# Performance work log

Hardware: AMD Instinct MI355X
Metric: run time of the kernel (lower is better)

The kernel has to match this reference:

```python
import jax, jax.numpy as jnp
import numpy as np

B, T, C, H = 4, 2048, 1024, 16
HS = C // H  # head dim = 64
EPS = 1e-5


def _layernorm(h, w, b):
    m = jnp.mean(h, axis=-1, keepdims=True)
    v = jnp.mean(jnp.square(h - m), axis=-1, keepdims=True)
    return (h - m) * jax.lax.rsqrt(v + EPS) * w + b


def _quantize_int8(t):
    # per-tensor absmax int8 quantization, matching the torch code
    absmax = jnp.max(jnp.abs(t))
    scale = jnp.where(absmax > 0, absmax / 127.0, jnp.float32(1.0))
    q = jnp.clip(jnp.round(t / scale), -127, 127).astype(jnp.int8)
    return q, scale


def setup_inputs() -> dict:
    key = jax.random.key(0)
    ks = jax.random.split(key, 8)
    w = lambda k, shape: (jax.random.normal(k, shape, jnp.float32) * 0.02)
    return {
        "x": jax.random.normal(ks[0], (B, T, C), jnp.float32),
        "ln1_w": jnp.ones((C,), jnp.float32),
        "ln1_b": jnp.zeros((C,), jnp.float32),
        "W_qkv": w(ks[1], (C, 3 * C)),
        "b_qkv": jnp.zeros((3 * C,), jnp.float32),
        "W_o": w(ks[2], (C, C)),
        "b_o": jnp.zeros((C,), jnp.float32),
        "ln2_w": jnp.ones((C,), jnp.float32),
        "ln2_b": jnp.zeros((C,), jnp.float32),
        "W_fc": w(ks[3], (C, 4 * C)),
        "b_fc": jnp.zeros((4 * C,), jnp.float32),
        "W_pr": w(ks[4], (4 * C, C)),
        "b_pr": jnp.zeros((C,), jnp.float32),
    }


def reference(x, ln1_w, ln1_b, W_qkv, b_qkv, W_o, b_o, ln2_w, ln2_b, W_fc, b_fc, W_pr, b_pr):
    # ---- attention (prefill, cache-owner, kv_cache_quant=True, use_cache=True) ----
    h = _layernorm(x, ln1_w, ln1_b)
    qkv = h @ W_qkv + b_qkv                       # (B,T,3C)
    q, k, v = jnp.split(qkv, 3, axis=-1)
    q = q.reshape(B, T, H, HS).transpose(0, 2, 1, 3)  # (B,H,T,hs)
    k = k.reshape(B, T, H, HS).transpose(0, 2, 1, 3)
    v = v.reshape(B, T, H, HS).transpose(0, 2, 1, 3)

    # quantized `present` cache (returned, not used for attention in prefill path)
    k_quant, k_scale = _quantize_int8(k)
    v_quant, v_scale = _quantize_int8(v)

    # causal SDPA (dropout=0)
    att = jnp.einsum("bhqd,bhkd->bhqk", q, k) * (1.0 / np.sqrt(HS))
    causal = jnp.tril(jnp.ones((T, T), bool))
    att = jnp.where(causal[None, None], att, jnp.float32(-jnp.inf))
    att = jax.nn.softmax(att, axis=-1)
    y = jnp.einsum("bhqk,bhkd->bhqd", att, v)
    y = y.transpose(0, 2, 1, 3).reshape(B, T, C)
    y = y @ W_o + b_o
    x = x + y

    # ---- MLP ----
    h2 = _layernorm(x, ln2_w, ln2_b)
    h2 = jax.nn.gelu(h2 @ W_fc + b_fc, approximate=False)
    x = x + (h2 @ W_pr + b_pr)

    return x, k_quant, k_scale, v_quant, v_scale
```

## Files before the change

kernel.cpp:

```cpp
#include <hip/hip_runtime.h>
#include <cmath>

typedef __bf16 bf16;
typedef float f32x4 __attribute__((ext_vector_type(4)));
typedef __bf16 bf16x4 __attribute__((ext_vector_type(4)));
typedef __bf16 bf16x8 __attribute__((ext_vector_type(8)));

#define DEVI __device__ __forceinline__

constexpr int Bn = 4, Tn = 2048, Cn = 1024, Hn = 16, HSn = 64;
constexpr int C3n = 3 * Cn;
constexpr int BTn = Bn * Tn;

constexpr size_t OFF_WT_QKV = 0;
constexpr size_t OFF_WT_O   = 6291456;
constexpr size_t OFF_WT_FC  = 8388608;
constexpr size_t OFF_WT_PR  = 16777216;
constexpr size_t OFF_H      = 25165824;
constexpr size_t OFF_Y      = 41943040;
constexpr size_t OFF_X1     = 58720256;
constexpr size_t OFF_AMAX   = 92274688;
constexpr size_t OFF_QKV    = 92274944;
constexpr size_t OFF_G      = OFF_QKV;

constexpr size_t OUT_X  = 0;
constexpr size_t OUT_KQ = 8388608;
constexpr size_t OUT_KS = 16777216;
constexpr size_t OUT_VQ = 16777217;
constexpr size_t OUT_VS = 25165825;

DEVI void g2l16(const void* g, void* l) {
  __builtin_amdgcn_global_load_lds(
      (__attribute__((address_space(1))) void*)g,
      (__attribute__((address_space(3))) void*)l, 16, 0, 0);
}

DEVI float gelu_f(float x) {
  const float ax = fabsf(x) * 0.7071067811865476f;
  const float t = 1.0f / (1.0f + 0.3275911f * ax);
  const float p = t * (0.254829592f + t * (-0.284496736f +
                  t * (1.421413741f + t * (-1.453152027f + t * 1.061405429f))));
  float er = 1.0f - p * __expf(-ax * ax);
  er = (x < 0.0f) ? -er : er;
  return 0.5f * x * (1.0f + er);
}

__global__ __launch_bounds__(256) void k_transpose(const float* __restrict__ W,
                                                   bf16* __restrict__ Wt,
                                                   int K, int N) {
  __shared__ float tile[32][33];
  const int n0 = blockIdx.x * 32, k0 = blockIdx.y * 32;
  const int tx = threadIdx.x, ty = threadIdx.y;
#pragma unroll
  for (int i = 0; i < 4; ++i) {
    int k = k0 + ty + i * 8;
    tile[ty + i * 8][tx] = W[(size_t)k * N + (n0 + tx)];
  }
  __syncthreads();
#pragma unroll
  for (int i = 0; i < 4; ++i) {
    int n = n0 + ty + i * 8;
    Wt[(size_t)n * K + (k0 + tx)] = (bf16)tile[tx][ty + i * 8];
  }
}

__global__ __launch_bounds__(256) void k_ln(const float* __restrict__ x,
                                            const float* __restrict__ g,
                                            const float* __restrict__ b,
                                            bf16* __restrict__ out) {
  __shared__ float red[8];
  const int row = blockIdx.x, tid = threadIdx.x;
  const int lane = tid & 63, wv = tid >> 6;
  f32x4 v = ((const f32x4*)(x + (size_t)row * Cn))[tid];

  float s = v[0] + v[1] + v[2] + v[3];
  s += __shfl_down(s, 32); s += __shfl_down(s, 16); s += __shfl_down(s, 8);
  s += __shfl_down(s, 4);  s += __shfl_down(s, 2);  s += __shfl_down(s, 1);
  if (!lane) red[wv] = s;
  __syncthreads();
  const float mean = (red[0] + red[1] + red[2] + red[3]) * (1.0f / 1024.0f);
  __syncthreads();

  f32x4 d = v - mean;
  float s2 = d[0]*d[0] + d[1]*d[1] + d[2]*d[2] + d[3]*d[3];
  s2 += __shfl_down(s2, 32); s2 += __shfl_down(s2, 16); s2 += __shfl_down(s2, 8);
  s2 += __shfl_down(s2, 4);  s2 += __shfl_down(s2, 2);  s2 += __shfl_down(s2, 1);
  if (!lane) red[wv] = s2;
  __syncthreads();
  const float var = (red[0] + red[1] + red[2] + red[3]) * (1.0f / 1024.0f);
  const float inv = rsqrtf(var + 1e-5f);

  f32x4 gw = ((const f32x4*)g)[tid];
  f32x4 bb = ((const f32x4*)b)[tid];
  bf16x4 o;
#pragma unroll
  for (int j = 0; j < 4; ++j) o[j] = (bf16)(d[j] * inv * gw[j] + bb[j]);
  *(bf16x4*)(out + (size_t)row * Cn + tid * 4) = o;
}

#define VMBAR(N) asm volatile("s_waitcnt vmcnt(" #N ")\n\ts_barrier" ::: "memory")
#define BARW()   asm volatile("s_barrier" ::: "memory")

DEVI void stage_half(const bf16* __restrict__ G, int ldk, int row0, int k0,
                     bf16* dst, int w, int lane) {
  const int srow = lane >> 3;
  const int sch = ((lane & 7) ^ srow) * 8;
  const bf16* src = G + (size_t)(row0 + srow) * ldk + k0 + sch;
#pragma unroll
  for (int i = 0; i < 2; ++i) {
    const int g = 2 * w + i;
    g2l16(src + (size_t)(8 * g) * ldk, dst + g * 512);
  }
}

DEVI void read_b(const bf16* BsB, int wn, int l15, int quad, bf16x8 (&bv)[4][2]) {
#pragma unroll
  for (int nt = 0; nt < 4; ++nt)
#pragma unroll
    for (int kk = 0; kk < 2; ++kk) {
      const int row = wn * 64 + nt * 16 + l15;
      const int c = ((kk * 4 + quad) ^ (l15 & 7)) * 8;
      bv[nt][kk] = *(const bf16x8*)(BsB + row * 64 + c);
    }
}

template <int MR, int Q>
DEVI void read_aq(const bf16* AsB, int wm, int l15, int quad, bf16x8 (&af)[MR][2]) {
#pragma unroll
  for (int r = 0; r < MR; ++r)
#pragma unroll
    for (int kk = 0; kk < 2; ++kk) {
      const int row = wm * (MR * 64) + (Q * MR + r) * 16 + l15;
      const int c = ((kk * 4 + quad) ^ (l15 & 7)) * 8;
      af[r][kk] = *(const bf16x8*)(AsB + row * 64 + c);
    }
}

template <int MR, int MF, int Q>
DEVI void mfma_q(const bf16x8 (&af)[MR][2], const bf16x8 (&bv)[4][2],
                 f32x4 (&acc)[MF][4]) {
  __builtin_amdgcn_s_setprio(1);
#pragma unroll
  for (int r = 0; r < MR; ++r)
#pragma unroll
    for (int nt = 0; nt < 4; ++nt)
#pragma unroll
      for (int kk = 0; kk < 2; ++kk)
        acc[Q * MR + r][nt] = __builtin_amdgcn_mfma_f32_16x16x32_bf16(
            af[r][kk], bv[nt][kk], acc[Q * MR + r][nt], 0, 0, 0);
  __builtin_amdgcn_s_setprio(0);
}

template <int BM, bool RES, bool GELU, bool AMAX, bool F32OUT>
__global__ __launch_bounds__(512, 2) void k_gemm256(const bf16* __restrict__ A,
                                                    const bf16* __restrict__ Bt,
                                                    const float* __restrict__ bias,
                                                    const float* __restrict__ res,
                                                    void* __restrict__ Cout,
                                                    unsigned int* __restrict__ amax,
                                                    int M, int N, int K) {
  constexpr int MR = BM / 128;
  constexpr int MF = BM / 32;
  __shared__ bf16 As[2][BM * 64];
  __shared__ bf16 Bs[2][256 * 64];
  __shared__ float redA[8];
  const int tid = threadIdx.x;
  const int lane = tid & 63, w = tid >> 6;
  const int wm = w >> 2, wn = w & 3;
  const int l15 = lane & 15, quad = lane >> 4;
  const int m0 = blockIdx.x * BM, n0 = blockIdx.y * 256;
  const int kIters = K >> 6, kLast = kIters - 1;
  (void)M;

#pragma unroll
  for (int hA = 0; hA < MR; ++hA)
    stage_half(A, K, m0 + 128 * hA, 0, As[0] + 8192 * hA, w, lane);
  stage_half(Bt, K, n0 + 0,   0,  Bs[0] + 0,    w, lane);
  stage_half(Bt, K, n0 + 128, 0,  Bs[0] + 8192, w, lane);
  stage_half(Bt, K, n0 + 0,   64, Bs[1] + 0,    w, lane);
  stage_half(Bt, K, n0 + 128, 64, Bs[1] + 8192, w, lane);

  f32x4 acc[MF][4] = {};

  for (int kt = 0; kt < kIters; ++kt) {
    const bf16* AsB = As[kt & 1];
    const bf16* BsB = Bs[kt & 1];
    bf16* AsN = As[(kt & 1) ^ 1];
    bf16* BsC = Bs[kt & 1];
    const bool stA = (kt + 1 < kIters);
    const bool stB = (kt + 2 < kIters);
    bf16x8 bv[4][2];
    bf16x8 af[MR][2];

    if (kt == kLast) { VMBAR(0); } else { VMBAR(4); }
    read_b(BsB, wn, l15, quad, bv);
    read_aq<MR, 0>(AsB, wm, l15, quad, af);
    if (stA) stage_half(A, K, m0 + 0, (kt + 1) * 64, AsN + 0, w, lane);
    mfma_q<MR, MF, 0>(af, bv, acc);

    BARW();
    read_aq<MR, 1>(AsB, wm, l15, quad, af);
    if constexpr (BM == 256) {
      if (stA) stage_half(A, K, m0 + 128, (kt + 1) * 64, AsN + 8192, w, lane);
    }
    mfma_q<MR, MF, 1>(af, bv, acc);

    BARW();
    read_aq<MR, 2>(AsB, wm, l15, quad, af);
    if (stB) stage_half(Bt, K, n0 + 0, (kt + 2) * 64, BsC + 0, w, lane);
    mfma_q<MR, MF, 2>(af, bv, acc);

    BARW();
    read_aq<MR, 3>(AsB, wm, l15, quad, af);
    if (stB) stage_half(Bt, K, n0 + 128, (kt + 2) * 64, BsC + 8192, w, lane);
    mfma_q<MR, MF, 3>(af, bv, acc);
  }

  const int colB = n0 + wn * 64 + l15;
  const int rowB = m0 + wm * (BM / 2) + (quad << 2);
  float lm = 0.0f;
#pragma unroll
  for (int mt = 0; mt < MF; ++mt) {
#pragma unroll
    for (int nt = 0; nt < 4; ++nt) {
      const int col = colB + nt * 16;
      const float bval = bias[col];
#pragma unroll
      for (int r = 0; r < 4; ++r) {
        const int row = rowB + mt * 16 + r;
        float val = acc[mt][nt][r] + bval;
        if (GELU) val = gelu_f(val);
        if (RES)  val += res[(size_t)row * N + col];
        if (AMAX) lm = fmaxf(lm, fabsf(val));
        if (F32OUT) ((float*)Cout)[(size_t)row * N + col] = val;
        else        ((bf16*)Cout)[(size_t)row * N + col] = (bf16)val;
      }
    }
  }

  if (AMAX) {
    const int cls = n0 >> 10;
    if (cls > 0) {
      lm = fmaxf(lm, __shfl_xor(lm, 1));
      lm = fmaxf(lm, __shfl_xor(lm, 2));
      lm = fmaxf(lm, __shfl_xor(lm, 4));
      lm = fmaxf(lm, __shfl_xor(lm, 8));
      lm = fmaxf(lm, __shfl_xor(lm, 16));
      lm = fmaxf(lm, __shfl_xor(lm, 32));
      if (!lane) redA[w] = lm;
      __syncthreads();
      if (tid == 0) {
        float m8 = redA[0];
#pragma unroll
        for (int i = 1; i < 8; ++i) m8 = fmaxf(m8, redA[i]);
        atomicMax(amax + (cls - 1), __float_as_uint(m8));
      }
    }
  }
}

__global__ __launch_bounds__(256) void k_init(unsigned int* amax) {
  if (threadIdx.x < 2) amax[threadIdx.x] = 0u;
}

__global__ __launch_bounds__(256) void k_quant(const bf16* __restrict__ qkv,
                                               const unsigned int* __restrict__ amax,
                                               float* __restrict__ out) {
  const float ka = __uint_as_float(amax[0]);
  const float va = __uint_as_float(amax[1]);
  const float ks = ka > 0.0f ? ka / 127.0f : 1.0f;
  const float vs = va > 0.0f ? va / 127.0f : 1.0f;
  if (blockIdx.x == 0 && threadIdx.x == 0) { out[OUT_KS] = ks; out[OUT_VS] = vs; }
  const float kinv = 1.0f / ks, vinv = 1.0f / vs;
  const size_t nchunks = 1048576;
  const size_t stride = (size_t)gridDim.x * blockDim.x;
  for (size_t ci = (size_t)blockIdx.x * blockDim.x + threadIdx.x; ci < nchunks; ci += stride) {
    const int d0 = (int)(ci & 7) * 8;
    const int t  = (int)(ci >> 3) & 2047;
    const int h  = (int)(ci >> 14) & 15;
    const int b  = (int)(ci >> 18);
    const size_t src = ((size_t)(b * Tn + t)) * C3n + h * HSn + d0;
    bf16x8 k8 = *(const bf16x8*)(qkv + src + Cn);
    bf16x8 v8 = *(const bf16x8*)(qkv + src + 2 * Cn);
    float kq[8], vq[8];
#pragma unroll
    for (int j = 0; j < 8; ++j) {
      kq[j] = fminf(fmaxf(rintf((float)k8[j] * kinv), -127.0f), 127.0f);
      vq[j] = fminf(fmaxf(rintf((float)v8[j] * vinv), -127.0f), 127.0f);
    }
    const size_t oi = ci * 8;
    f32x4 a0 = {kq[0], kq[1], kq[2], kq[3]};
    f32x4 a1 = {kq[4], kq[5], kq[6], kq[7]};
    *(f32x4*)(out + OUT_KQ + oi)     = a0;
    *(f32x4*)(out + OUT_KQ + oi + 4) = a1;
    float* vdst = out + OUT_VQ + oi;
#pragma unroll
    for (int j = 0; j < 8; ++j) vdst[j] = vq[j];
  }
}

__global__ __launch_bounds__(256, 3) void k_attn(const bf16* __restrict__ qkv,
                                                 bf16* __restrict__ y) {
  __shared__ bf16 Ks[2][64 * 64];
  __shared__ bf16 Vt[2][64 * 64];
  __shared__ bf16 Pt[4][2][16 * 64];

  const int tid = threadIdx.x;
  const int lane = tid & 63;
  const int w = tid >> 6;
  const int quad = lane >> 4;
  const int l15 = lane & 15;

  const int bh = blockIdx.x;
  const int qt = 15 - (int)blockIdx.y;
  const int b = bh >> 4, h = bh & 15;
  const int q0 = qt * 128;
  const int ktMax = 2 * qt + 1;

  const bf16* qkv_b = qkv + (size_t)b * Tn * C3n + h * HSn;
  const bf16* kbase = qkv_b + Cn;
  const bf16* vbase = qkv_b + 2 * Cn;

  const int srow = lane >> 3;
  const int schunk = ((lane & 7) ^ srow) * 8;

  const bf16* q0p = qkv_b + (size_t)(q0 + 16 * w + l15) * C3n;
  const bf16* q1p = q0p + (size_t)64 * C3n;
  bf16x8 qf[2][2];
  qf[0][0] = *(const bf16x8*)(q0p + quad * 8);
  qf[0][1] = *(const bf16x8*)(q0p + 32 + quad * 8);
  qf[1][0] = *(const bf16x8*)(q1p + quad * 8);
  qf[1][1] = *(const bf16x8*)(q1p + 32 + quad * 8);

  g2l16(kbase + (size_t)(8 * w + srow) * C3n + schunk, (bf16*)Ks[0] + w * 512);
  g2l16(kbase + (size_t)(8 * (w + 4) + srow) * C3n + schunk, (bf16*)Ks[0] + (w + 4) * 512);
  bf16x8 v0 = *(const bf16x8*)(vbase + (size_t)lane * C3n + w * 8);
  bf16x8 v1 = *(const bf16x8*)(vbase + (size_t)lane * C3n + (w + 4) * 8);
  __builtin_amdgcn_s_waitcnt(0);
#pragma unroll
  for (int j = 0; j < 8; ++j) {
    Vt[0][(w * 8 + j) * 64 + ((srow ^ j) << 3) + (lane & 7)] = v0[j];
    Vt[0][((w + 4) * 8 + j) * 64 + ((srow ^ j) << 3) + (lane & 7)] = v1[j];
  }
  __syncthreads();

  f32x4 Od[2][4] = {};
  float m_i[2] = {-INFINITY, -INFINITY};
  float l_i[2] = {0.0f, 0.0f};

  for (int kt = 0; kt <= ktMax; ++kt) {
    const int bsel = kt & 1;

    bf16x8 nv0, nv1;
    if (kt < ktMax) {
      const int kv1 = (kt + 1) * 64;
      g2l16(kbase + (size_t)(kv1 + 8 * w + srow) * C3n + schunk,
            (bf16*)Ks[bsel ^ 1] + w * 512);
      g2l16(kbase + (size_t)(kv1 + 8 * (w + 4) + srow) * C3n + schunk,
            (bf16*)Ks[bsel ^ 1] + (w + 4) * 512);
      nv0 = *(const bf16x8*)(vbase + (size_t)(kv1 + lane) * C3n + w * 8);
      nv1 = *(const bf16x8*)(vbase + (size_t)(kv1 + lane) * C3n + (w + 4) * 8);
    }

    const bf16* KsB = Ks[bsel];
    f32x4 S0[4] = {}, S1[4] = {};
#pragma unroll
    for (int ks = 0; ks < 2; ++ks)
#pragma unroll
      for (int nt = 0; nt < 4; ++nt) {
        const int rn = nt * 16 + l15;
        const int c = ((ks * 4 + quad) ^ (l15 & 7)) * 8;
        bf16x8 kf = *(const bf16x8*)(KsB + rn * 64 + c);
        S0[nt] = __builtin_amdgcn_mfma_f32_16x16x32_bf16(kf, qf[0][ks], S0[nt], 0, 0, 0);
        S1[nt] = __builtin_amdgcn_mfma_f32_16x16x32_bf16(kf, qf[1][ks], S1[nt], 0, 0, 0);
      }

    const int qloc = 16 * w + l15;
    const int th[2] = { kt < 2 * qt ? 64 : (kt == 2 * qt ? qloc : -1),
                        kt < ktMax ? 64 : qloc };
    f32x4* Sg[2] = {S0, S1};
#pragma unroll
    for (int g = 0; g < 2; ++g) {
      float s[4][4];
      float mx = -INFINITY;
#pragma unroll
      for (int nt = 0; nt < 4; ++nt)
#pragma unroll
        for (int r = 0; r < 4; ++r) {
          float v = Sg[g][nt][r] * 0.125f;
          if (nt * 16 + quad * 4 + r > th[g]) v = -INFINITY;
          s[nt][r] = v;
          mx = fmaxf(mx, v);
        }
      mx = fmaxf(mx, __shfl_xor(mx, 16));
      mx = fmaxf(mx, __shfl_xor(mx, 32));
      const float mn = fmaxf(m_i[g], mx);
      const float al = __expf(m_i[g] - mn);
      m_i[g] = mn;
      float rsum = 0.0f;
      bf16x4 pk[4];
#pragma unroll
      for (int nt = 0; nt < 4; ++nt)
#pragma unroll
        for (int r = 0; r < 4; ++r) {
          const float p = __expf(s[nt][r] - mn);
          rsum += p;
          pk[nt][r] = (bf16)p;
        }
      rsum += __shfl_xor(rsum, 16);
      rsum += __shfl_xor(rsum, 32);
      l_i[g] = l_i[g] * al + rsum;
#pragma unroll
      for (int dt = 0; dt < 4; ++dt) Od[g][dt] *= al;
#pragma unroll
      for (int nt = 0; nt < 4; ++nt) {
        const int phys = (nt * 2 + (quad >> 1)) ^ (l15 & 7);
        *(bf16x4*)(&Pt[w][g][0] + l15 * 64 + phys * 8 + (quad & 1) * 4) = pk[nt];
      }
    }

    const bf16* VtB = Vt[bsel];
#pragma unroll
    for (int ks2 = 0; ks2 < 2; ++ks2) {
      const int pc = ((ks2 * 4 + quad) ^ (l15 & 7)) * 8;
      bf16x8 pf0 = *(const bf16x8*)(&Pt[w][0][0] + l15 * 64 + pc);
      bf16x8 pf1 = *(const bf16x8*)(&Pt[w][1][0] + l15 * 64 + pc);
#pragma unroll
      for (int dt = 0; dt < 4; ++dt) {
        const int d = dt * 16 + l15;
        bf16x8 vf = *(const bf16x8*)(VtB + d * 64 + pc);
        Od[0][dt] = __builtin_amdgcn_mfma_f32_16x16x32_bf16(vf, pf0, Od[0][dt], 0, 0, 0);
        Od[1][dt] = __builtin_amdgcn_mfma_f32_16x16x32_bf16(vf, pf1, Od[1][dt], 0, 0, 0);
      }
    }

    if (kt < ktMax) {
      __builtin_amdgcn_s_waitcnt(0);
#pragma unroll
      for (int j = 0; j < 8; ++j) {
        Vt[bsel ^ 1][(w * 8 + j) * 64 + ((srow ^ j) << 3) + (lane & 7)] = nv0[j];
        Vt[bsel ^ 1][((w + 4) * 8 + j) * 64 + ((srow ^ j) << 3) + (lane & 7)] = nv1[j];
      }
      __syncthreads();
    }
  }

#pragma unroll
  for (int g = 0; g < 2; ++g) {
    const float invl = 1.0f / l_i[g];
    const size_t yb = ((size_t)b * Tn + q0 + g * 64 + 16 * w + l15) * Cn + h * HSn;
#pragma unroll
    for (int dt = 0; dt < 4; ++dt) {
      bf16x4 o;
#pragma unroll
      for (int r = 0; r < 4; ++r) o[r] = (bf16)(Od[g][dt][r] * invl);
      *(bf16x4*)(y + yb + dt * 16 + quad * 4) = o;
    }
  }
}

extern "C" void kernel_launch(void* const* d_in, const int* in_sizes, int n_in,
                              void* d_out, int out_size, void* d_ws, size_t ws_size,
                              hipStream_t stream) {
  const float* x     = (const float*)d_in[0];
  const float* ln1w  = (const float*)d_in[1];
  const float* ln1b  = (const float*)d_in[2];
  const float* Wqkv  = (const float*)d_in[3];
  const float* bqkv  = (const float*)d_in[4];
  const float* Wo    = (const float*)d_in[5];
  const float* bo    = (const float*)d_in[6];
  const float* ln2w  = (const float*)d_in[7];
  const float* ln2b  = (const float*)d_in[8];
  const float* Wfc   = (const float*)d_in[9];
  const float* bfc   = (const float*)d_in[10];
  const float* Wpr   = (const float*)d_in[11];
  const float* bpr   = (const float*)d_in[12];

  char* ws = (char*)d_ws;
  bf16*  Wt_qkv = (bf16*)(ws + OFF_WT_QKV);
  bf16*  Wt_o   = (bf16*)(ws + OFF_WT_O);
  bf16*  Wt_fc  = (bf16*)(ws + OFF_WT_FC);
  bf16*  Wt_pr  = (bf16*)(ws + OFF_WT_PR);
  bf16*  h      = (bf16*)(ws + OFF_H);
  bf16*  ybf    = (bf16*)(ws + OFF_Y);
  float* x1     = (float*)(ws + OFF_X1);
  unsigned int* amax = (unsigned int*)(ws + OFF_AMAX);
  bf16*  qkvbf  = (bf16*)(ws + OFF_QKV);
  bf16*  g      = (bf16*)(ws + OFF_G);
  float* out    = (float*)d_out;

  const dim3 tb(32, 8);
  k_transpose<<<dim3(96, 32),  tb, 0, stream>>>(Wqkv, Wt_qkv, 1024, 3072);
  k_transpose<<<dim3(32, 32),  tb, 0, stream>>>(Wo,   Wt_o,   1024, 1024);
  k_transpose<<<dim3(128, 32), tb, 0, stream>>>(Wfc,  Wt_fc,  1024, 4096);
  k_transpose<<<dim3(32, 128), tb, 0, stream>>>(Wpr,  Wt_pr,  4096, 1024);
  k_init<<<1, 64, 0, stream>>>(amax);

  k_ln<<<BTn, 256, 0, stream>>>(x, ln1w, ln1b, h);
  k_gemm256<256, false, false, true, false><<<dim3(32, 12), 512, 0, stream>>>(
      h, Wt_qkv, bqkv, nullptr, qkvbf, amax, 8192, 3072, 1024);
  k_quant<<<2048, 256, 0, stream>>>(qkvbf, amax, out);
  k_attn<<<dim3(64, 16), 256, 0, stream>>>(qkvbf, ybf);
  k_gemm256<128, true, false, false, true><<<dim3(64, 4), 512, 0, stream>>>(
      ybf, Wt_o, bo, x, x1, nullptr, 8192, 1024, 1024);
  k_ln<<<BTn, 256, 0, stream>>>(x1, ln2w, ln2b, h);
  k_gemm256<256, false, true, false, false><<<dim3(32, 16), 512, 0, stream>>>(
      h, Wt_fc, bfc, nullptr, g, nullptr, 8192, 4096, 1024);
  k_gemm256<128, true, false, false, true><<<dim3(64, 4), 512, 0, stream>>>(
      g, Wt_pr, bpr, x1, out, nullptr, 8192, 1024, 4096);
}
```

Before: 546.5 us.

## Restructure GEMM main loop into two-stage prefetch with fewer barriers per k-tile

Rewrites the GEMM k-loop so each k-tile reads all A fragments and B from LDS up front, then issues global-to-LDS staging of tile kt+2 into the buffer just consumed. This cuts the barriers per iteration from four to two. The loop is unrolled in pairs with compile-time buffer selection, and sched_barrier and explicit vmcnt/lgkmcnt waits control instruction order. It trades more live registers for the extra fragment sets against less synchronization. It also assumes an even number of k-iterations.

Result: faster. 533.2 us (-2.4%).

```diff
diff --git a/kernel.cpp b/kernel.cpp
--- a/kernel.cpp
+++ b/kernel.cpp
@@ -98,8 +98,10 @@
   *(bf16x4*)(out + (size_t)row * Cn + tid * 4) = o;
 }
 
-#define VMBAR(N) asm volatile("s_waitcnt vmcnt(" #N ")\n\ts_barrier" ::: "memory")
+#define VMCNT(N) asm volatile("s_waitcnt vmcnt(" #N ")" ::: "memory")
+#define LGKM0()  asm volatile("s_waitcnt lgkmcnt(0)" ::: "memory")
 #define BARW()   asm volatile("s_barrier" ::: "memory")
+#define SCHEDB() __builtin_amdgcn_sched_barrier(0)
 
 DEVI void stage_half(const bf16* __restrict__ G, int ldk, int row0, int k0,
                      bf16* dst, int w, int lane) {
@@ -149,6 +151,55 @@
         acc[Q * MR + r][nt] = __builtin_amdgcn_mfma_f32_16x16x32_bf16(
             af[r][kk], bv[nt][kk], acc[Q * MR + r][nt], 0, 0, 0);
   __builtin_amdgcn_s_setprio(0);
+}
+
+template <int BM, int BUF>
+DEVI void tile_iter(int kt, int kIters, const bf16* __restrict__ A,
+                    const bf16* __restrict__ Bt, int K, int m0, int n0,
+                    bf16* As0, bf16* As1, bf16* Bs0, bf16* Bs1,
+                    f32x4 (&acc)[BM / 32][4], int w, int lane) {
+  constexpr int MR = BM / 128, MF = BM / 32;
+  const int l15 = lane & 15, quad = lane >> 4;
+  const int wm = w >> 2, wn = w & 3;
+  const bf16* AsB = BUF ? As1 : As0;
+  const bf16* BsB = BUF ? Bs1 : Bs0;
+  bf16* AsW = BUF ? As1 : As0;
+  bf16* BsW = BUF ? Bs1 : Bs0;
+
+  bf16x8 bv[4][2];
+  bf16x8 af0[MR][2], af1[MR][2], af2[MR][2], af3[MR][2];
+
+  read_b(BsB, wn, l15, quad, bv);
+  read_aq<MR, 0>(AsB, wm, l15, quad, af0);
+  read_aq<MR, 1>(AsB, wm, l15, quad, af1);
+  LGKM0(); SCHEDB();
+  mfma_q<MR, MF, 0>(af0, bv, acc);
+  SCHEDB();
+
+  read_aq<MR, 2>(AsB, wm, l15, quad, af2);
+  read_aq<MR, 3>(AsB, wm, l15, quad, af3);
+  LGKM0(); SCHEDB();
+  mfma_q<MR, MF, 1>(af1, bv, acc);
+  SCHEDB();
+  BARW();
+
+  if (kt + 2 < kIters) {
+    stage_half(A, K, m0 + 0, (kt + 2) * 64, AsW + 0, w, lane);
+    if constexpr (BM == 256)
+      stage_half(A, K, m0 + 128, (kt + 2) * 64, AsW + 8192, w, lane);
+    stage_half(Bt, K, n0 + 0,   (kt + 2) * 64, BsW + 0,    w, lane);
+    stage_half(Bt, K, n0 + 128, (kt + 2) * 64, BsW + 8192, w, lane);
+  }
+  mfma_q<MR, MF, 2>(af2, bv, acc);
+  mfma_q<MR, MF, 3>(af3, bv, acc);
+  SCHEDB();
+  if (kt + 2 < kIters) {
+    if constexpr (BM == 256) { VMCNT(8); } else { VMCNT(6); }
+    BARW();
+  } else if (kt + 1 < kIters) {
+    VMCNT(0);
+    BARW();
+  }
 }
 
 template <int BM, bool RES, bool GELU, bool AMAX, bool F32OUT>
@@ -161,59 +212,34 @@
                                                     int M, int N, int K) {
   constexpr int MR = BM / 128;
   constexpr int MF = BM / 32;
-  __shared__ bf16 As[2][BM * 64];
-  __shared__ bf16 Bs[2][256 * 64];
+  __shared__ bf16 As0[BM * 64], As1[BM * 64];
+  __shared__ bf16 Bs0[256 * 64], Bs1[256 * 64];
   __shared__ float redA[8];
   const int tid = threadIdx.x;
   const int lane = tid & 63, w = tid >> 6;
   const int wm = w >> 2, wn = w & 3;
   const int l15 = lane & 15, quad = lane >> 4;
   const int m0 = blockIdx.x * BM, n0 = blockIdx.y * 256;
-  const int kIters = K >> 6, kLast = kIters - 1;
+  const int kIters = K >> 6;
   (void)M;
 
-#pragma unroll
-  for (int hA = 0; hA < MR; ++hA)
-    stage_half(A, K, m0 + 128 * hA, 0, As[0] + 8192 * hA, w, lane);
-  stage_half(Bt, K, n0 + 0,   0,  Bs[0] + 0,    w, lane);
-  stage_half(Bt, K, n0 + 128, 0,  Bs[0] + 8192, w, lane);
-  stage_half(Bt, K, n0 + 0,   64, Bs[1] + 0,    w, lane);
-  stage_half(Bt, K, n0 + 128, 64, Bs[1] + 8192, w, lane);
+  stage_half(A, K, m0 + 0, 0, As0 + 0, w, lane);
+  if constexpr (BM == 256) stage_half(A, K, m0 + 128, 0, As0 + 8192, w, lane);
+  stage_half(Bt, K, n0 + 0,   0, Bs0 + 0,    w, lane);
+  stage_half(Bt, K, n0 + 128, 0, Bs0 + 8192, w, lane);
+  stage_half(A, K, m0 + 0, 64, As1 + 0, w, lane);
+  if constexpr (BM == 256) stage_half(A, K, m0 + 128, 64, As1 + 8192, w, lane);
+  stage_half(Bt, K, n0 + 0,   64, Bs1 + 0,    w, lane);
+  stage_half(Bt, K, n0 + 128, 64, Bs1 + 8192, w, lane);
+  if constexpr (BM == 256) { VMCNT(8); } else { VMCNT(6); }
+  BARW();
 
   f32x4 acc[MF][4] = {};
 
-  for (int kt = 0; kt < kIters; ++kt) {
-    const bf16* AsB = As[kt & 1];
-    const bf16* BsB = Bs[kt & 1];
-    bf16* AsN = As[(kt & 1) ^ 1];
-    bf16* BsC = Bs[kt & 1];
-    const bool stA = (kt + 1 < kIters);
-    const bool stB = (kt + 2 < kIters);
-    bf16x8 bv[4][2];
-    bf16x8 af[MR][2];
-
-    if (kt == kLast) { VMBAR(0); } else { VMBAR(4); }
-    read_b(BsB, wn, l15, quad, bv);
-    read_aq<MR, 0>(AsB, wm, l15, quad, af);
-    if (stA) stage_half(A, K, m0 + 0, (kt + 1) * 64, AsN + 0, w, lane);
-    mfma_q<MR, MF, 0>(af, bv, acc);
-
-    BARW();
-    read_aq<MR, 1>(AsB, wm, l15, quad, af);
-    if constexpr (BM == 256) {
-      if (stA) stage_half(A, K, m0 + 128, (kt + 1) * 64, AsN + 8192, w, lane);
-    }
-    mfma_q<MR, MF, 1>(af, bv, acc);
-
-    BARW();
-    read_aq<MR, 2>(AsB, wm, l15, quad, af);
-    if (stB) stage_half(Bt, K, n0 + 0, (kt + 2) * 64, BsC + 0, w, lane);
-    mfma_q<MR, MF, 2>(af, bv, acc);
-
-    BARW();
-    read_aq<MR, 3>(AsB, wm, l15, quad, af);
-    if (stB) stage_half(Bt, K, n0 + 128, (kt + 2) * 64, BsC + 8192, w, lane);
-    mfma_q<MR, MF, 3>(af, bv, acc);
+  const int nPairs = kIters >> 1;
+  for (int p = 0; p < nPairs; ++p) {
+    tile_iter<BM, 0>(2 * p,     kIters, A, Bt, K, m0, n0, As0, As1, Bs0, Bs1, acc, w, lane);
+    tile_iter<BM, 1>(2 * p + 1, kIters, A, Bt, K, m0, n0, As0, As1, Bs0, Bs1, acc, w, lane);
   }
 
   const int colB = n0 + wn * 64 + l15;
```
